# Performance work log

Hardware: AMD Instinct MI355X
Metric: run time of the kernel (lower is better)

## Reference

```python
import jax, jax.numpy as jnp
import numpy as np

B, S, D, F, E, K = 4, 2048, 512, 1024, 8, 2

def setup_inputs() -> dict:
    key = jax.random.key(0)
    ks = jax.random.split(key, 7)
    hidden = jax.random.normal(ks[0], (B, S, D), dtype=jnp.float32)
    top_k_indices = jax.random.randint(ks[1], (B, S, K), 0, E, dtype=jnp.int32)
    top_k_weights = jax.random.uniform(ks[2], (B, S, K), dtype=jnp.float32)
    scale1 = 1.0 / np.sqrt(D)
    scale2 = 1.0 / np.sqrt(F)
    W1 = jax.random.normal(ks[3], (E, D, F), dtype=jnp.float32) * scale1
    b1 = jnp.zeros((E, F), dtype=jnp.float32)
    W2 = jax.random.normal(ks[4], (E, F, D), dtype=jnp.float32) * scale2
    b2 = jnp.zeros((E, D), dtype=jnp.float32)
    return {"hidden": hidden, "top_k_indices": top_k_indices,
            "top_k_weights": top_k_weights, "W1": W1, "b1": b1, "W2": W2, "b2": b2}

def reference(hidden, top_k_indices, top_k_weights, W1, b1, W2, b2):
    b, s, d = hidden.shape
    e = W1.shape[0]
    x = hidden.reshape(-1, d)                      # [T, D]
    idx = top_k_indices.reshape(-1, top_k_indices.shape[-1])   # [T, K]
    w = top_k_weights.reshape(-1, top_k_weights.shape[-1])     # [T, K]
    # combine weight per (token, expert): sum over k slots routed to expert e
    onehot = jax.nn.one_hot(idx, e, dtype=w.dtype)             # [T, K, E]
    cw = jnp.einsum('tk,tke->et', w, onehot)                   # [E, T]
    def step(acc, params):
        W1e, b1e, W2e, b2e, cwe = params
        h = jax.nn.gelu(x @ W1e + b1e)                         # [T, F]
        y = h @ W2e + b2e                                      # [T, D]
        return acc + cwe[:, None] * y, None
    out, _ = jax.lax.scan(step, jnp.zeros_like(x), (W1, b1, W2, b2, cw))
    return out.reshape(b, s, d)
```

## Files before the change

kernel.cpp:

```cpp
#include <hip/hip_runtime.h>
#include <hip/hip_bf16.h>

#define T_TOK 8192
#define DDIM  512
#define FDIM  1024
#define NEXP  8
#define KTOP  2
#define NSLOT (T_TOK * KTOP)
#define MAX_ROWS 17408
#define MAX_T128 136

#define NB_CAST 512
#define NB_T    4096
#define PREP_BLOCKS (1 + NB_CAST + NB_T + NB_T)

typedef __attribute__((ext_vector_type(8))) __bf16 bf16x8;
typedef __attribute__((ext_vector_type(4))) __bf16 bf16x4;
typedef __attribute__((ext_vector_type(4))) float  f32x4;
typedef __attribute__((ext_vector_type(8))) unsigned short u16x8;

typedef __attribute__((address_space(1))) const unsigned int* gp1;
typedef __attribute__((address_space(3))) unsigned int*       lp3;
#define GL2LDS(g, l) __builtin_amdgcn_global_load_lds((gp1)(const void*)(g), (lp3)(void*)(l), 16, 0, 0)


__device__ __forceinline__ float gelu_fast(float x){
    float u = 0.7978845608028654f * (x + 0.044715f * x * x * x);
    return x / (1.0f + __expf(-2.0f * u));
}

__device__ __forceinline__ unsigned short f2bf(float v){
    __hip_bfloat16 b = __float2bfloat16(v);
    return *(unsigned short*)&b;
}

__global__ __launch_bounds__(1024) void prep_kernel(
    const float* __restrict__ x, const int* __restrict__ idx,
    const float* __restrict__ W1, const float* __restrict__ W2,
    unsigned short* __restrict__ xbf,
    unsigned short* __restrict__ w1t, unsigned short* __restrict__ w2t,
    int* __restrict__ meta, int2* __restrict__ map,
    int* __restrict__ list, int* __restrict__ slot2row)
{
    __shared__ unsigned long long sA[1024], sB[1024];
    __shared__ unsigned short tile[32][33];
    const int b   = blockIdx.x;
    const int tid = threadIdx.x;

    if (b == 0){
        const int base = tid * 16;
        int mye[16];
        unsigned long long a = 0, bb = 0;
        #pragma unroll
        for (int i = 0; i < 16; i++){
            int e = idx[base + i] & 7;
            mye[i] = e;
            unsigned long long one = 1ull << (16 * (e & 3));
            if (e < 4) a += one; else bb += one;
        }
        sA[tid] = a; sB[tid] = bb;
        __syncthreads();
        for (int off = 1; off < 1024; off <<= 1){
            unsigned long long ta = 0, tb = 0;
            if (tid >= off){ ta = sA[tid - off]; tb = sB[tid - off]; }
            __syncthreads();
            sA[tid] += ta; sB[tid] += tb;
            __syncthreads();
        }
        const unsigned long long iA = sA[tid],  iB = sB[tid];
        const unsigned long long tA = sA[1023], tB = sB[1023];

        int cnt[NEXP], pad[NEXP], off_e[NEXP], tc[NEXP + 1];
        tc[0] = 0;
        int o = 0;
        #pragma unroll
        for (int e = 0; e < NEXP; e++){
            unsigned long long src = (e < 4) ? tA : tB;
            cnt[e] = (int)((src >> (16 * (e & 3))) & 0xffffull);
            pad[e] = (cnt[e] + 127) & ~127;
            off_e[e] = o; o += pad[e];
            tc[e + 1] = tc[e] + (pad[e] >> 7);
        }
        const int nrows = o, nt = tc[NEXP];

        if (tid == 0) meta[16] = nt;
        if (tid < NEXP) meta[17 + tid] = off_e[tid];
        if (tid < nt){
            int e = 0;
            while (tid >= tc[e + 1]) e++;
            map[tid] = make_int2(e, off_e[e] + (tid - tc[e]) * 128);
        }

        int run[NEXP];
        #pragma unroll
        for (int e = 0; e < NEXP; e++){
            unsigned long long isrc = (e < 4) ? iA : iB;
            unsigned long long csrc = (e < 4) ? a  : bb;
            int incl = (int)((isrc >> (16 * (e & 3))) & 0xffffull);
            int ce   = (int)((csrc >> (16 * (e & 3))) & 0xffffull);
            run[e] = off_e[e] + incl - ce;
        }
        #pragma unroll
        for (int i = 0; i < 16; i++){
            int e = mye[i];
            int gg = run[e]++;
            list[gg] = (base + i) >> 1;
            slot2row[base + i] = gg;
        }
        for (int p = tid; p < nrows; p += 1024){
            #pragma unroll
            for (int e = 0; e < NEXP; e++){
                if (p >= off_e[e] + cnt[e] && p < off_e[e] + pad[e]) list[p] = 0;
            }
        }
    } else if (b < 1 + NB_CAST){
        int i = (b - 1) * 1024 + tid;
        const float4* s = (const float4*)x;
        float4 va = s[2 * i];
        float4 vb = s[2 * i + 1];
        u16x8 ov;
        ov[0] = f2bf(va.x); ov[1] = f2bf(va.y); ov[2] = f2bf(va.z); ov[3] = f2bf(va.w);
        ov[4] = f2bf(vb.x); ov[5] = f2bf(vb.y); ov[6] = f2bf(vb.z); ov[7] = f2bf(vb.w);
        *(u16x8*)(xbf + (size_t)i * 8) = ov;
    } else {
        int blk = b - (1 + NB_CAST);
        const float* src; unsigned short* dst; int R, C, cpb_shift, cpb_mask;
        if (blk < NB_T){ src = W1; dst = w1t; R = DDIM; C = FDIM; cpb_shift = 5; cpb_mask = 31; }
        else           { src = W2; dst = w2t; R = FDIM; C = DDIM; cpb_shift = 4; cpb_mask = 15; blk -= NB_T; }
        int e   = blk >> 9;
        int rem = blk & 511;
        int rb  = rem >> cpb_shift, cb = rem & cpb_mask;
        int r0 = rb * 32, c0 = cb * 32;
        int tx = tid & 31, ty = tid >> 5;
        const float* sf = src + (size_t)e * R * C;
        unsigned short* d = dst + (size_t)e * R * C;
        tile[ty][tx] = f2bf(sf[(size_t)(r0 + ty) * C + c0 + tx]);
        __syncthreads();
        d[(size_t)(c0 + ty) * R + r0 + tx] = tile[tx][ty];
    }
}

#define PIPE_SYNC() do {                                             \
    asm volatile("s_waitcnt vmcnt(0)" ::: "memory");                 \
    __builtin_amdgcn_s_barrier();                                    \
    __builtin_amdgcn_sched_barrier(0);                               \
} while (0)

__global__ __launch_bounds__(256) void gemm1_kernel(
    const unsigned short* __restrict__ x,
    const unsigned short* __restrict__ w1t,
    const float* __restrict__ b1,
    const int* __restrict__ meta,
    const int2* __restrict__ map,
    const int* __restrict__ list,
    unsigned short* __restrict__ h)
{
    const int ntiles = meta[16];
    const int nwg = ntiles * (FDIM / 128);
    int id = blockIdx.y * gridDim.x + blockIdx.x;
    if (id >= nwg) return;
    int q = nwg >> 3, r = nwg & 7;
    int xcd = id & 7, rank = id >> 3;
    int swz = (xcd < r) ? (xcd * (q + 1) + rank)
                        : (r * (q + 1) + (xcd - r) * q + rank);
    const int tile = swz >> 3;
    const int n0 = (swz & 7) * 128;
    int2 em = map[tile];
    const int e = em.x, grow0 = em.y;

    __shared__ __align__(16) unsigned short As[2][128 * 32];
    __shared__ __align__(16) unsigned short Bs[2][128 * 32];

    const int tid  = threadIdx.x;
    const int wave = tid >> 6;
    const int lane = tid & 63;
    const int rl   = lane >> 2;
    const int kq   = lane & 3;

    const int row0 = wave * 16 + rl;
    const int row1 = 64 + wave * 16 + rl;

    const unsigned short* pA0 = x + (size_t)list[grow0 + row0] * DDIM + kq * 8;
    const unsigned short* pA1 = x + (size_t)list[grow0 + row1] * DDIM + kq * 8;
    const unsigned short* pB0 = w1t + ((size_t)e * FDIM + n0 + row0) * DDIM + kq * 8;
    const unsigned short* pB1 = w1t + ((size_t)e * FDIM + n0 + row1) * DDIM + kq * 8;

    const int quad = lane >> 4, lrow = lane & 15;
    const int wr = (wave >> 1) * 64;
    const int wc = (wave & 1) * 64;

#define STG1(buf, kk) do {                                            \
        char* la_ = (char*)As[buf] + wave * 1024;                     \
        char* lb_ = (char*)Bs[buf] + wave * 1024;                     \
        GL2LDS(pA0 + (kk), la_);  GL2LDS(pA1 + (kk), la_ + 4096);     \
        GL2LDS(pB0 + (kk), lb_);  GL2LDS(pB1 + (kk), lb_ + 4096);     \
    } while (0)

    f32x4 acc[4][4];
    #pragma unroll
    for (int i = 0; i < 4; i++)
        #pragma unroll
        for (int j = 0; j < 4; j++) acc[i][j] = (f32x4)0.0f;

    STG1(0, 0);
    PIPE_SYNC();

    const int NK = DDIM / 32;
    #pragma unroll 2
    for (int t = 0; t < NK; ++t){
        const int cur = t & 1;
        if (t + 1 < NK) STG1(cur ^ 1, (t + 1) * 32);
        bf16x8 a[4], b[4];
        #pragma unroll
        for (int i = 0; i < 4; i++){
            a[i] = *(const bf16x8*)&As[cur][(wr + i * 16 + lrow) * 32 + quad * 8];
            b[i] = *(const bf16x8*)&Bs[cur][(wc + i * 16 + lrow) * 32 + quad * 8];
        }
        #pragma unroll
        for (int i = 0; i < 4; i++)
            #pragma unroll
            for (int j = 0; j < 4; j++)
                acc[i][j] = __builtin_amdgcn_mfma_f32_16x16x32_bf16(a[i], b[j], acc[i][j], 0, 0, 0);
        if (t + 1 < NK) PIPE_SYNC();
    }
#undef STG1

    #pragma unroll
    for (int j = 0; j < 4; j++){
        int cn = n0 + wc + j * 16 + lrow;
        float bias = b1[e * FDIM + cn];
        #pragma unroll
        for (int i = 0; i < 4; i++){
            #pragma unroll
            for (int rr = 0; rr < 4; rr++){
                int gr = grow0 + wr + i * 16 + quad * 4 + rr;
                h[(size_t)gr * FDIM + cn] = f2bf(gelu_fast(acc[i][j][rr] + bias));
            }
        }
    }
}

__global__ __launch_bounds__(256) void gemm2_kernel(
    const unsigned short* __restrict__ h,
    const unsigned short* __restrict__ w2t,
    const float* __restrict__ b2,
    const int* __restrict__ meta,
    const int2* __restrict__ map,
    unsigned short* __restrict__ y)
{
    const int ntiles = meta[16];
    const int nwg = ntiles * (DDIM / 128);
    int id = blockIdx.y * gridDim.x + blockIdx.x;
    if (id >= nwg) return;
    int q = nwg >> 3, r = nwg & 7;
    int xcd = id & 7, rank = id >> 3;
    int swz = (xcd < r) ? (xcd * (q + 1) + rank)
                        : (r * (q + 1) + (xcd - r) * q + rank);
    const int tile = swz >> 2;
    const int n0 = (swz & 3) * 128;
    int2 em = map[tile];
    const int e = em.x, grow0 = em.y;

    __shared__ __align__(16) unsigned short As[2][128 * 32];
    __shared__ __align__(16) unsigned short Bs[2][128 * 32];

    const int tid  = threadIdx.x;
    const int wave = tid >> 6;
    const int lane = tid & 63;
    const int rl   = lane >> 2;
    const int kq   = lane & 3;

    const int row0 = wave * 16 + rl;
    const int row1 = 64 + wave * 16 + rl;

    const unsigned short* pA0 = h + (size_t)(grow0 + row0) * FDIM + kq * 8;
    const unsigned short* pA1 = h + (size_t)(grow0 + row1) * FDIM + kq * 8;
    const unsigned short* pB0 = w2t + ((size_t)e * DDIM + n0 + row0) * FDIM + kq * 8;
    const unsigned short* pB1 = w2t + ((size_t)e * DDIM + n0 + row1) * FDIM + kq * 8;

    const int quad = lane >> 4, lrow = lane & 15;
    const int wr = (wave >> 1) * 64;
    const int wc = (wave & 1) * 64;

#define STG2(buf, kk) do {                                            \
        char* la_ = (char*)As[buf] + wave * 1024;                     \
        char* lb_ = (char*)Bs[buf] + wave * 1024;                     \
        GL2LDS(pA0 + (kk), la_);  GL2LDS(pA1 + (kk), la_ + 4096);     \
        GL2LDS(pB0 + (kk), lb_);  GL2LDS(pB1 + (kk), lb_ + 4096);     \
    } while (0)

    f32x4 acc[4][4];
    #pragma unroll
    for (int i = 0; i < 4; i++)
        #pragma unroll
        for (int j = 0; j < 4; j++) acc[i][j] = (f32x4)0.0f;

    STG2(0, 0);
    PIPE_SYNC();

    const int NK = FDIM / 32;
    #pragma unroll 2
    for (int t = 0; t < NK; ++t){
        const int cur = t & 1;
        if (t + 1 < NK) STG2(cur ^ 1, (t + 1) * 32);
        bf16x8 a[4], b[4];
        #pragma unroll
        for (int i = 0; i < 4; i++){
            a[i] = *(const bf16x8*)&As[cur][(wr + i * 16 + lrow) * 32 + quad * 8];
            b[i] = *(const bf16x8*)&Bs[cur][(wc + i * 16 + lrow) * 32 + quad * 8];
        }
        #pragma unroll
        for (int i = 0; i < 4; i++)
            #pragma unroll
            for (int j = 0; j < 4; j++)
                acc[i][j] = __builtin_amdgcn_mfma_f32_16x16x32_bf16(a[i], b[j], acc[i][j], 0, 0, 0);
        if (t + 1 < NK) PIPE_SYNC();
    }
#undef STG2

    #pragma unroll
    for (int j = 0; j < 4; j++){
        int cn = n0 + wc + j * 16 + lrow;
        float bias = b2[e * DDIM + cn];
        #pragma unroll
        for (int i = 0; i < 4; i++){
            #pragma unroll
            for (int rr = 0; rr < 4; rr++){
                int gr = grow0 + wr + i * 16 + quad * 4 + rr;
                y[(size_t)gr * DDIM + cn] = f2bf(acc[i][j][rr] + bias);
            }
        }
    }
}

__global__ void combine_kernel(const unsigned short* __restrict__ y,
                               const int* __restrict__ slot2row,
                               const float* __restrict__ wk,
                               float* __restrict__ out){
    int g = blockIdx.x * blockDim.x + threadIdx.x;
    int t = g >> 7, seg = g & 127;
    int ra = slot2row[2 * t], rb = slot2row[2 * t + 1];
    float wa = wk[2 * t];
    float wb = wk[2 * t + 1];
    bf16x4 ya = *(const bf16x4*)(y + (size_t)ra * DDIM + seg * 4);
    bf16x4 yb = *(const bf16x4*)(y + (size_t)rb * DDIM + seg * 4);
    float4 o;
    o.x = wa * (float)ya[0] + wb * (float)yb[0];
    o.y = wa * (float)ya[1] + wb * (float)yb[1];
    o.z = wa * (float)ya[2] + wb * (float)yb[2];
    o.w = wa * (float)ya[3] + wb * (float)yb[3];
    *(float4*)(out + (size_t)t * DDIM + seg * 4) = o;
}

extern "C" void kernel_launch(void* const* d_in, const int* in_sizes, int n_in,
                              void* d_out, int out_size, void* d_ws, size_t ws_size,
                              hipStream_t stream){
    const float* x   = (const float*)d_in[0];
    const int*   idx = (const int*)d_in[1];
    const float* wk  = (const float*)d_in[2];
    const float* W1  = (const float*)d_in[3];
    const float* b1  = (const float*)d_in[4];
    const float* W2  = (const float*)d_in[5];
    const float* b2  = (const float*)d_in[6];
    float* out = (float*)d_out;

    char* ws = (char*)d_ws;
    int*   meta     = (int*)ws;
    int2*  map      = (int2*)(ws + 512);
    int*   list     = (int*)(ws + 4096);
    int*   slot2row = (int*)(ws + 81920);
    unsigned short* xbf = (unsigned short*)(ws + 262144);
    unsigned short* w1t = (unsigned short*)(ws + 8650752);
    unsigned short* w2t = (unsigned short*)(ws + 17039360);
    unsigned short* h   = (unsigned short*)(ws + 25427968);
    unsigned short* y   = (unsigned short*)(ws + 61079552);
    if (ws_size < 78905344u) return;

    prep_kernel<<<PREP_BLOCKS, 1024, 0, stream>>>(
        x, idx, W1, W2, xbf, w1t, w2t, meta, map, list, slot2row);

    gemm1_kernel<<<dim3(FDIM / 128, MAX_T128), 256, 0, stream>>>(
        xbf, w1t, b1, meta, map, list, h);

    gemm2_kernel<<<dim3(DDIM / 128, MAX_T128), 256, 0, stream>>>(
        h, w2t, b2, meta, map, y);

    combine_kernel<<<(T_TOK * DDIM / 4) / 256, 256, 0, stream>>>(y, slot2row, wk, out);
}
```

Baseline: 210.3 us.

## Deepen GEMM K-tile to 64 with partial vmcnt waits and occupancy hint

Both expert GEMM kernels now stage K-tiles of 64 instead of 32 into two explicit LDS buffer sets. Each stage waits only until the previous tile's loads have landed (vmcnt(8)), so the next tile's global-to-LDS copies stay in flight during compute. This halves the number of barriers per K element and keeps more loads outstanding. LDS use doubles to 64KB per block, and launch_bounds(256,2) asks for two blocks per CU, which may raise register pressure.

```diff
diff --git a/kernel.cpp b/kernel.cpp
--- a/kernel.cpp
+++ b/kernel.cpp
@@ -140,13 +140,23 @@
     }
 }
 
-#define PIPE_SYNC() do {                                             \
+#define WAIT8_BAR() do {                                             \
+    asm volatile("s_waitcnt vmcnt(8)" ::: "memory");                 \
+    __builtin_amdgcn_s_barrier();                                    \
+    __builtin_amdgcn_sched_barrier(0);                               \
+} while (0)
+#define WAIT0_BAR() do {                                             \
     asm volatile("s_waitcnt vmcnt(0)" ::: "memory");                 \
     __builtin_amdgcn_s_barrier();                                    \
     __builtin_amdgcn_sched_barrier(0);                               \
 } while (0)
-
-__global__ __launch_bounds__(256) void gemm1_kernel(
+#define POST_BAR() do {                                              \
+    __builtin_amdgcn_sched_barrier(0);                               \
+    __builtin_amdgcn_s_barrier();                                    \
+    __builtin_amdgcn_sched_barrier(0);                               \
+} while (0)
+
+__global__ __launch_bounds__(256, 2) void gemm1_kernel(
     const unsigned short* __restrict__ x,
     const unsigned short* __restrict__ w1t,
     const float* __restrict__ b1,
@@ -168,8 +178,10 @@
     int2 em = map[tile];
     const int e = em.x, grow0 = em.y;
 
-    __shared__ __align__(16) unsigned short As[2][128 * 32];
-    __shared__ __align__(16) unsigned short Bs[2][128 * 32];
+    __shared__ __align__(16) unsigned short As0[2 * 128 * 32];
+    __shared__ __align__(16) unsigned short As1[2 * 128 * 32];
+    __shared__ __align__(16) unsigned short Bs0[2 * 128 * 32];
+    __shared__ __align__(16) unsigned short Bs1[2 * 128 * 32];
 
     const int tid  = threadIdx.x;
     const int wave = tid >> 6;
@@ -189,11 +201,33 @@
     const int wr = (wave >> 1) * 64;
     const int wc = (wave & 1) * 64;
 
-#define STG1(buf, kk) do {                                            \
-        char* la_ = (char*)As[buf] + wave * 1024;                     \
-        char* lb_ = (char*)Bs[buf] + wave * 1024;                     \
-        GL2LDS(pA0 + (kk), la_);  GL2LDS(pA1 + (kk), la_ + 4096);     \
-        GL2LDS(pB0 + (kk), lb_);  GL2LDS(pB1 + (kk), lb_ + 4096);     \
+#define STG(AS, BS, kk) do {                                          \
+        char* la_ = (char*)(AS) + wave * 1024;                        \
+        char* lb_ = (char*)(BS) + wave * 1024;                        \
+        GL2LDS(pA0 + (kk),      la_);          GL2LDS(pA1 + (kk),      la_ + 4096);  \
+        GL2LDS(pA0 + (kk) + 32, la_ + 8192);   GL2LDS(pA1 + (kk) + 32, la_ + 12288); \
+        GL2LDS(pB0 + (kk),      lb_);          GL2LDS(pB1 + (kk),      lb_ + 4096);  \
+        GL2LDS(pB0 + (kk) + 32, lb_ + 8192);   GL2LDS(pB1 + (kk) + 32, lb_ + 12288); \
+    } while (0)
+
+#define CMP(AS, BS) do {                                              \
+        bf16x8 a_[4][2], b_[4][2];                                    \
+        _Pragma("unroll")                                             \
+        for (int i = 0; i < 4; i++){                                  \
+            _Pragma("unroll")                                         \
+            for (int ks = 0; ks < 2; ks++){                           \
+                a_[i][ks] = *(const bf16x8*)&(AS)[ks * 4096 + (wr + i * 16 + lrow) * 32 + quad * 8]; \
+                b_[i][ks] = *(const bf16x8*)&(BS)[ks * 4096 + (wc + i * 16 + lrow) * 32 + quad * 8]; \
+            }                                                         \
+        }                                                             \
+        _Pragma("unroll")                                             \
+        for (int i = 0; i < 4; i++){                                  \
+            _Pragma("unroll")                                         \
+            for (int j = 0; j < 4; j++){                              \
+                acc[i][j] = __builtin_amdgcn_mfma_f32_16x16x32_bf16(a_[i][0], b_[j][0], acc[i][j], 0, 0, 0); \
+                acc[i][j] = __builtin_amdgcn_mfma_f32_16x16x32_bf16(a_[i][1], b_[j][1], acc[i][j], 0, 0, 0); \
+            }                                                         \
+        }                                                             \
     } while (0)
 
     f32x4 acc[4][4];
@@ -202,28 +236,24 @@
         #pragma unroll
         for (int j = 0; j < 4; j++) acc[i][j] = (f32x4)0.0f;
 
-    STG1(0, 0);
-    PIPE_SYNC();
-
-    const int NK = DDIM / 32;
-    #pragma unroll 2
-    for (int t = 0; t < NK; ++t){
-        const int cur = t & 1;
-        if (t + 1 < NK) STG1(cur ^ 1, (t + 1) * 32);
-        bf16x8 a[4], b[4];
-        #pragma unroll
-        for (int i = 0; i < 4; i++){
-            a[i] = *(const bf16x8*)&As[cur][(wr + i * 16 + lrow) * 32 + quad * 8];
-            b[i] = *(const bf16x8*)&Bs[cur][(wc + i * 16 + lrow) * 32 + quad * 8];
-        }
-        #pragma unroll
-        for (int i = 0; i < 4; i++)
-            #pragma unroll
-            for (int j = 0; j < 4; j++)
-                acc[i][j] = __builtin_amdgcn_mfma_f32_16x16x32_bf16(a[i], b[j], acc[i][j], 0, 0, 0);
-        if (t + 1 < NK) PIPE_SYNC();
+    STG(As0, Bs0, 0);
+    const int NK = DDIM / 64;
+    for (int t = 0; t < NK; t += 2){
+        STG(As1, Bs1, (t + 1) * 64);
+        WAIT8_BAR();
+        CMP(As0, Bs0);
+        POST_BAR();
+        if (t + 2 < NK){
+            STG(As0, Bs0, (t + 2) * 64);
+            WAIT8_BAR();
+        } else {
+            WAIT0_BAR();
+        }
+        CMP(As1, Bs1);
+        POST_BAR();
     }
-#undef STG1
+#undef STG
+#undef CMP
 
     #pragma unroll
     for (int j = 0; j < 4; j++){
@@ -240,7 +270,7 @@
     }
 }
 
-__global__ __launch_bounds__(256) void gemm2_kernel(
+__global__ __launch_bounds__(256, 2) void gemm2_kernel(
     const unsigned short* __restrict__ h,
     const unsigned short* __restrict__ w2t,
     const float* __restrict__ b2,
@@ -261,8 +291,10 @@
     int2 em = map[tile];
     const int e = em.x, grow0 = em.y;
 
-    __shared__ __align__(16) unsigned short As[2][128 * 32];
-    __shared__ __align__(16) unsigned short Bs[2][128 * 32];
+    __shared__ __align__(16) unsigned short As0[2 * 128 * 32];
+    __shared__ __align__(16) unsigned short As1[2 * 128 * 32];
+    __shared__ __align__(16) unsigned short Bs0[2 * 128 * 32];
+    __shared__ __align__(16) unsigned short Bs1[2 * 128 * 32];
 
     const int tid  = threadIdx.x;
     const int wave = tid >> 6;
@@ -282,11 +314,33 @@
     const int wr = (wave >> 1) * 64;
     const int wc = (wave & 1) * 64;
 
-#define STG2(buf, kk) do {                                            \
-        char* la_ = (char*)As[buf] + wave * 1024;                     \
-        char* lb_ = (char*)Bs[buf] + wave * 1024;                     \
-        GL2LDS(pA0 + (kk), la_);  GL2LDS(pA1 + (kk), la_ + 4096);     \
-        GL2LDS(pB0 + (kk), lb_);  GL2LDS(pB1 + (kk), lb_ + 4096);     \
+#define STG(AS, BS, kk) do {                                          \
+        char* la_ = (char*)(AS) + wave * 1024;                        \
+        char* lb_ = (char*)(BS) + wave * 1024;                        \
+        GL2LDS(pA0 + (kk),      la_);          GL2LDS(pA1 + (kk),      la_ + 4096);  \
+        GL2LDS(pA0 + (kk) + 32, la_ + 8192);   GL2LDS(pA1 + (kk) + 32, la_ + 12288); \
+        GL2LDS(pB0 + (kk),      lb_);          GL2LDS(pB1 + (kk),      lb_ + 4096);  \
+        GL2LDS(pB0 + (kk) + 32, lb_ + 8192);   GL2LDS(pB1 + (kk) + 32, lb_ + 12288); \
+    } while (0)
+
+#define CMP(AS, BS) do {                                              \
+        bf16x8 a_[4][2], b_[4][2];                                    \
+        _Pragma("unroll")                                             \
+        for (int i = 0; i < 4; i++){                                  \
+            _Pragma("unroll")                                         \
+            for (int ks = 0; ks < 2; ks++){                           \
+                a_[i][ks] = *(const bf16x8*)&(AS)[ks * 4096 + (wr + i * 16 + lrow) * 32 + quad * 8]; \
+                b_[i][ks] = *(const bf16x8*)&(BS)[ks * 4096 + (wc + i * 16 + lrow) * 32 + quad * 8]; \
+            }                                                         \
+        }                                                             \
+        _Pragma("unroll")                                             \
+        for (int i = 0; i < 4; i++){                                  \
+            _Pragma("unroll")                                         \
+            for (int j = 0; j < 4; j++){                              \
+                acc[i][j] = __builtin_amdgcn_mfma_f32_16x16x32_bf16(a_[i][0], b_[j][0], acc[i][j], 0, 0, 0); \
+                acc[i][j] = __builtin_amdgcn_mfma_f32_16x16x32_bf16(a_[i][1], b_[j][1], acc[i][j], 0, 0, 0); \
+            }                                                         \
+        }                                                             \
     } while (0)
 
     f32x4 acc[4][4];
@@ -295,28 +349,24 @@
         #pragma unroll
         for (int j = 0; j < 4; j++) acc[i][j] = (f32x4)0.0f;
 
-    STG2(0, 0);
-    PIPE_SYNC();
-
-    const int NK = FDIM / 32;
-    #pragma unroll 2
-    for (int t = 0; t < NK; ++t){
-        const int cur = t & 1;
-        if (t + 1 < NK) STG2(cur ^ 1, (t + 1) * 32);
-        bf16x8 a[4], b[4];
-        #pragma unroll
-        for (int i = 0; i < 4; i++){
-            a[i] = *(const bf16x8*)&As[cur][(wr + i * 16 + lrow) * 32 + quad * 8];
-            b[i] = *(const bf16x8*)&Bs[cur][(wc + i * 16 + lrow) * 32 + quad * 8];
-        }
-        #pragma unroll
-        for (int i = 0; i < 4; i++)
-            #pragma unroll
-            for (int j = 0; j < 4; j++)
-                acc[i][j] = __builtin_amdgcn_mfma_f32_16x16x32_bf16(a[i], b[j], acc[i][j], 0, 0, 0);
-        if (t + 1 < NK) PIPE_SYNC();
+    STG(As0, Bs0, 0);
+    const int NK = FDIM / 64;
+    for (int t = 0; t < NK; t += 2){
+        STG(As1, Bs1, (t + 1) * 64);
+        WAIT8_BAR();
+        CMP(As0, Bs0);
+        POST_BAR();
+        if (t + 2 < NK){
+            STG(As0, Bs0, (t + 2) * 64);
+            WAIT8_BAR();
+        } else {
+            WAIT0_BAR();
+        }
+        CMP(As1, Bs1);
+        POST_BAR();
     }
-#undef STG2
+#undef STG
+#undef CMP
 
     #pragma unroll
     for (int j = 0; j < 4; j++){
```

Result: faster. 187.9 us (-10.6%).
